# Performance work log

Hardware: AMD Instinct MI355X
Metric: run time of the kernel (lower is better)

Reference implementation:

```python
import jax, jax.numpy as jnp
import numpy as np

NMS_PRE_MAXSIZE = 4096
NMS_POST_MAXSIZE = 512
NMS_THRESH = 0.7


def setup_inputs() -> dict:
    key = jax.random.key(0)
    k1, k2, k3, k4, k5 = jax.random.split(key, 5)
    B, N, C = 4, 32768, 3
    # realistic 3D boxes: (x, y, z, dx, dy, dz, heading)
    xy = jax.random.uniform(k1, (B, N, 2), dtype=jnp.float32) * 70.0
    z = jax.random.uniform(k2, (B, N, 1), dtype=jnp.float32) * 4.0 - 2.0
    sizes = jax.random.uniform(k3, (B, N, 3), dtype=jnp.float32) * 3.0 + 1.0
    heading = jax.random.uniform(k4, (B, N, 1), dtype=jnp.float32) * 6.2832 - 3.1416
    batch_box_preds = jnp.concatenate([xy, z, sizes, heading], axis=-1)  # (B,N,7)
    batch_cls_preds = jax.random.uniform(k5, (B, N, C), dtype=jnp.float32)  # (B,N,3)
    return {"batch_box_preds": batch_box_preds, "batch_cls_preds": batch_cls_preds}


def _nms_single(boxes, scores, labels):
    # boxes (N,7), scores (N,), labels (N,) int32
    top_s, idx = jax.lax.top_k(scores, NMS_PRE_MAXSIZE)   # sort desc, keep pre-maxsize
    b = boxes[idx]                                        # (PRE,7)
    l = labels[idx]
    # BEV axis-aligned IoU (reference surrogate for the rotated-BEV CUDA IoU kernel)
    x, y, dx, dy = b[:, 0], b[:, 1], b[:, 3], b[:, 4]
    x1, x2 = x - 0.5 * dx, x + 0.5 * dx
    y1, y2 = y - 0.5 * dy, y + 0.5 * dy
    area = dx * dy
    ix = jnp.maximum(0.0, jnp.minimum(x2[:, None], x2[None, :]) - jnp.maximum(x1[:, None], x1[None, :]))
    iy = jnp.maximum(0.0, jnp.minimum(y2[:, None], y2[None, :]) - jnp.maximum(y1[:, None], y1[None, :]))
    inter = ix * iy
    iou = jax.lax.stop_gradient(inter / (area[:, None] + area[None, :] - inter + 1e-6))

    ar = jnp.arange(NMS_PRE_MAXSIZE)

    def body(i, keep):
        sup = (iou[i] > NMS_THRESH) & (ar > i) & keep[i]
        return keep & ~sup

    keep = jax.lax.fori_loop(0, NMS_PRE_MAXSIZE, body, jnp.ones(NMS_PRE_MAXSIZE, bool))

    # pack first NMS_POST_MAXSIZE kept boxes into fixed-size zero-padded outputs
    rank = jnp.cumsum(keep) - 1
    valid = keep & (rank < NMS_POST_MAXSIZE)
    pos = jnp.where(valid, rank, NMS_POST_MAXSIZE)  # invalid -> scratch row
    rois = jnp.zeros((NMS_POST_MAXSIZE + 1, 7), b.dtype).at[pos].set(b)[:NMS_POST_MAXSIZE]
    sc = jnp.zeros((NMS_POST_MAXSIZE + 1,), top_s.dtype).at[pos].set(top_s)[:NMS_POST_MAXSIZE]
    lb = jnp.zeros((NMS_POST_MAXSIZE + 1,), jnp.int32).at[pos].set(l)[:NMS_POST_MAXSIZE]
    return rois, sc, lb


def reference(batch_box_preds, batch_cls_preds):
    # per-box max score / argmax class (torch.max(cls_preds, dim=1) per sample)
    roi_scores_all = jnp.max(batch_cls_preds, axis=-1)                 # (B,N)
    roi_labels_all = jnp.argmax(batch_cls_preds, axis=-1).astype(jnp.int32)
    rois, roi_scores, roi_labels = jax.vmap(_nms_single)(batch_box_preds, roi_scores_all, roi_labels_all)
    return rois, roi_scores, roi_labels + 1  # labels shifted by +1 as in proposal_layer
```

## Files before the change

kernel.cpp:

```cpp
#include <hip/hip_runtime.h>
#include <stdint.h>

#define BB 4
#define NN 32768
#define PRE 4096
#define POST 512
#define NMS_TH 0.7f
#define MIDCAP 8192
#define P1G 10
#define T1 595
#define T2 1485

typedef unsigned long long u64;
typedef unsigned int u32;

__device__ __forceinline__ u32 orderable(float f) {
  u32 u = __float_as_uint(f);
  return (u & 0x80000000u) ? ~u : (u | 0x80000000u);
}
__device__ __forceinline__ float unorderable(u32 o) {
  u32 u = (o & 0x80000000u) ? (o & 0x7fffffffu) : ~o;
  return __uint_as_float(u);
}
__device__ __forceinline__ u32 bucket_of(float s) {
  u32 v = (u32)(s * 2147483648.0f);
  u32 bk = v >> 20;
  return bk > 2047u ? 2047u : bk;
}
__device__ __forceinline__ u64 readlane64(u64 v, int l) {
  u32 lo = (u32)__builtin_amdgcn_readlane((int)(u32)v, l);
  u32 hi = (u32)__builtin_amdgcn_readlane((int)(u32)(v >> 32), l);
  return ((u64)hi << 32) | lo;
}

__global__ void zero_kernel(u32* __restrict__ hist, u32* __restrict__ cnt_mid,
                            u64* __restrict__ rowAnyBm) {
  int t = blockIdx.x * 256 + threadIdx.x;
  if (t < BB * 2048) hist[t] = 0;
  if (t < BB * 64) rowAnyBm[t] = 0;
  if (t < BB) cnt_mid[t] = 0;
}

__global__ __launch_bounds__(256) void score_hist_kernel(const float* __restrict__ cls,
                                                         int* __restrict__ labels,
                                                         u64* __restrict__ keys,
                                                         u32* __restrict__ hist) {
  __shared__ u32 lh[2048];
  for (int t = threadIdx.x; t < 2048; t += 256) lh[t] = 0;
  __syncthreads();
  int t4 = blockIdx.x * 256 + threadIdx.x;
  int base4 = t4 * 4;
  const float4* c4 = (const float4*)(cls + (size_t)t4 * 12);
  float4 va = c4[0], vb = c4[1], vc = c4[2];
  float v[12] = {va.x, va.y, va.z, va.w, vb.x, vb.y, vb.z, vb.w, vc.x, vc.y, vc.z, vc.w};
  u64 ks[4]; int ls[4];
#pragma unroll
  for (int p = 0; p < 4; ++p) {
    float s = v[3 * p]; int l = 0;
    if (v[3 * p + 1] > s) { s = v[3 * p + 1]; l = 1; }
    if (v[3 * p + 2] > s) { s = v[3 * p + 2]; l = 2; }
    int n = (base4 + p) & (NN - 1);
    ks[p] = ((u64)orderable(s) << 32) | (u32)(~(u32)n);
    ls[p] = l;
    atomicAdd(&lh[bucket_of(s)], 1u);
  }
  *(ulonglong2*)(keys + base4) = make_ulonglong2(ks[0], ks[1]);
  *(ulonglong2*)(keys + base4 + 2) = make_ulonglong2(ks[2], ks[3]);
  *(int4*)(labels + base4) = make_int4(ls[0], ls[1], ls[2], ls[3]);
  __syncthreads();
  int b = blockIdx.x >> 5;
  for (int t = threadIdx.x; t < 2048; t += 256) {
    u32 vv = lh[t];
    if (vv) atomicAdd(&hist[b * 2048 + t], vv);
  }
}

__global__ __launch_bounds__(256) void select_kernel(const u32* __restrict__ hist,
                                                     u32* __restrict__ selinfo,
                                                     u32* __restrict__ sfxBuf,
                                                     u32* __restrict__ cursor) {
  __shared__ u32 sfx[2048];
  int b = blockIdx.x;
  for (int t = threadIdx.x; t < 2048; t += 256) sfx[t] = hist[b * 2048 + t];
  __syncthreads();
  for (int d = 1; d < 2048; d <<= 1) {
    u32 v[8];
#pragma unroll
    for (int i = 0; i < 8; ++i) {
      int t = threadIdx.x + i * 256;
      v[i] = (t + d < 2048) ? sfx[t + d] : 0;
    }
    __syncthreads();
#pragma unroll
    for (int i = 0; i < 8; ++i) sfx[threadIdx.x + i * 256] += v[i];
    __syncthreads();
  }
  for (int t = threadIdx.x; t < 2048; t += 256) {
    u32 above = (t + 1 < 2048) ? sfx[t + 1] : 0;
    sfxBuf[b * 2048 + t] = sfx[t];
    cursor[b * 2048 + t] = above;
    if (above < PRE && sfx[t] >= PRE) { selinfo[b * 2] = (u32)t; selinfo[b * 2 + 1] = above; }
  }
}

__global__ __launch_bounds__(256) void compact_kernel(const u64* __restrict__ keys,
                                                      const u32* __restrict__ selinfo,
                                                      u32* __restrict__ cursor,
                                                      u64* __restrict__ sel, u64* __restrict__ mid,
                                                      u32* __restrict__ cnt_mid) {
  int t4 = blockIdx.x * 256 + threadIdx.x;
  int base4 = t4 * 4;
  int b = base4 >> 15;
  u32 T = selinfo[b * 2];
  ulonglong2 k01 = *(const ulonglong2*)(keys + base4);
  ulonglong2 k23 = *(const ulonglong2*)(keys + base4 + 2);
  u64 kk[4] = {k01.x, k01.y, k23.x, k23.y};
#pragma unroll
  for (int p = 0; p < 4; ++p) {
    u64 key = kk[p];
    u32 bk = bucket_of(unorderable((u32)(key >> 32)));
    if (bk > T) {
      u32 q = atomicAdd(&cursor[b * 2048 + bk], 1u);
      sel[((size_t)b << 12) + q] = key;
    } else if (bk == T) {
      u32 q = atomicAdd(&cnt_mid[b], 1u);
      if (q < MIDCAP) mid[(size_t)b * MIDCAP + q] = key;
    }
  }
}

__global__ __launch_bounds__(64) void bsort_kernel(u64* __restrict__ sel, u64* __restrict__ mid,
                                                   const u32* __restrict__ sfxBuf,
                                                   const u32* __restrict__ selinfo,
                                                   const u32* __restrict__ cnt_mid,
                                                   const float* __restrict__ boxes,
                                                   const int* __restrict__ labels,
                                                   float* __restrict__ topBox,
                                                   float4* __restrict__ P,
                                                   float* __restrict__ AR,
                                                   float* __restrict__ topS,
                                                   int* __restrict__ topL) {
  int t = blockIdx.x & 2047;
  int b = blockIdx.x >> 11;
  int lane = threadIdx.x;
  u32 T = selinfo[b * 2];
  if ((u32)t < T) return;
  u64* selB = sel + ((size_t)b << 12);
  u32 start, end;
  if ((u32)t == T) {
    u32 C1 = selinfo[b * 2 + 1];
    int need = PRE - (int)C1;
    int M = (int)cnt_mid[b]; if (M > MIDCAP) M = MIDCAP;
    u64* midB = mid + (size_t)b * MIDCAP;
    for (int r = 0; r < need; ++r) {
      u64 best = 0; int bi = -1;
      for (int q = lane; q < M; q += 64) {
        u64 v = midB[q];
        if (v > best) { best = v; bi = q; }
      }
#pragma unroll
      for (int d = 32; d > 0; d >>= 1) {
        u64 ob = __shfl_xor(best, d, 64);
        int oi = __shfl_xor(bi, d, 64);
        if (ob > best) { best = ob; bi = oi; }
      }
      if (lane == 0) selB[C1 + r] = best;
      if (bi >= 0 && lane == (bi & 63)) midB[bi] = 0;
    }
    start = C1; end = PRE;
  } else {
    start = (t < 2047) ? sfxBuf[b * 2048 + t + 1] : 0u;
    end = sfxBuf[b * 2048 + t];
    int n = (int)(end - start);
    if (n > 64) {
      for (int r = 0; r < n - 1; ++r) {
        u64 best = 0; int bi = -1;
        for (int q = r + lane; q < n; q += 64) {
          u64 v = selB[start + q];
          if (v > best) { best = v; bi = q; }
        }
#pragma unroll
        for (int d = 32; d > 0; d >>= 1) {
          u64 ob = __shfl_xor(best, d, 64);
          int oi = __shfl_xor(bi, d, 64);
          if (ob > best) { best = ob; bi = oi; }
        }
        if (lane == 0) {
          u64 tmp = selB[start + r];
          selB[start + r] = best;
          selB[start + bi] = tmp;
        }
      }
    } else if (n > 1) {
      u64 v = (lane < n) ? selB[start + lane] : 0ULL;
#pragma unroll
      for (int k = 2; k <= 64; k <<= 1) {
#pragma unroll
        for (int j = k >> 1; j > 0; j >>= 1) {
          u64 o = __shfl_xor(v, j, 64);
          bool up = ((lane & k) == 0);
          bool first = ((lane & j) == 0);
          u64 mx = v > o ? v : o, mn = v > o ? o : v;
          v = (first == up) ? mx : mn;
        }
      }
      if (lane < n) selB[start + lane] = v;
    }
  }
  __builtin_amdgcn_s_waitcnt(0);
  for (u32 pos = start + lane; pos < end; pos += 64) {
    u64 key = selB[pos];
    u32 n = ~(u32)key;
    size_t src = (size_t)b * NN + n;
    const float* bx = boxes + src * 7;
    float x = bx[0], y = bx[1], dx = bx[3], dy = bx[4];
    size_t gidx = ((size_t)b << 12) + pos;
    float* tb = topBox + gidx * 7;
#pragma unroll
    for (int c = 0; c < 7; ++c) tb[c] = bx[c];
    float4 p;
    p.x = x - 0.5f * dx; p.z = x + 0.5f * dx;
    p.y = y - 0.5f * dy; p.w = y + 0.5f * dy;
    P[gidx] = p;
    AR[gidx] = dx * dy;
    topS[gidx] = unorderable((u32)(key >> 32));
    topL[gidx] = labels[src];
  }
}

__device__ __forceinline__ void mask_tile(int b, int rb, int w, int lane,
                                          const float4* __restrict__ P,
                                          const float* __restrict__ AR,
                                          u64* __restrict__ maskT,
                                          u64* __restrict__ diag,
                                          u64* __restrict__ rowAnyBm) {
  int base = b << 12;
  int row = (rb << 6) + lane;
  float4 rp = P[base + row];
  float rar = AR[base + row];
  const float4* __restrict__ Pcol = P + base + (w << 6);
  const float* __restrict__ ARcol = AR + base + (w << 6);
  u64 bits = 0;
  float margMin = 1.0f;
#pragma unroll 8
  for (int k = 0; k < 64; ++k) {
    float4 cb = Pcol[k];
    float ca = ARcol[k];
    float ix = fminf(rp.z, cb.z) - fmaxf(rp.x, cb.x); ix = fmaxf(0.0f, ix);
    float iy = fminf(rp.w, cb.w) - fmaxf(rp.y, cb.y); iy = fmaxf(0.0f, iy);
    float inter = ix * iy;
    float denom = ((rar + ca) - inter) + 1e-6f;
    float t = 0.7f * denom;
    bits |= ((u64)(inter > t ? 1u : 0u)) << k;
    margMin = fminf(margMin, fabsf(inter - t) - 2e-5f * t);
  }
  if (__any(margMin <= 0.0f)) {
    bits = 0;
    for (int k = 0; k < 64; ++k) {
      float4 cb = Pcol[k];
      float ca = ARcol[k];
      float ix = fminf(rp.z, cb.z) - fmaxf(rp.x, cb.x); ix = fmaxf(0.0f, ix);
      float iy = fminf(rp.w, cb.w) - fmaxf(rp.y, cb.y); iy = fmaxf(0.0f, iy);
      float inter = ix * iy;
      float denom = ((rar + ca) - inter) + 1e-6f;
      bits |= ((u64)(((inter / denom) > NMS_TH) ? 1u : 0u)) << k;
    }
  }
  maskT[((size_t)(b * 64 + w)) * PRE + row] = bits;
  if (w == rb) diag[base + row] = bits;
  else {
    u64 anyw = __ballot(bits != 0ULL);
    if (lane == 0 && anyw)
      atomicOr((unsigned long long*)&rowAnyBm[b * 64 + rb], anyw);
  }
}

__global__ __launch_bounds__(256) void mask1_kernel(const float4* __restrict__ P,
                                                    const float* __restrict__ AR,
                                                    u64* __restrict__ maskT,
                                                    u64* __restrict__ diag,
                                                    u64* __restrict__ rowAnyBm) {
  int b = blockIdx.y;
  int ti = blockIdx.x * 4 + (threadIdx.x >> 6);
  if (ti >= T1) return;
  int lane = threadIdx.x & 63;
  int rb = 0;
  while (rb < P1G - 1 && (64 * (rb + 1) - ((rb + 1) * rb) / 2) <= ti) ++rb;
  int w = rb + (ti - (64 * rb - (rb * (rb - 1)) / 2));
  mask_tile(b, rb, w, lane, P, AR, maskT, diag, rowAnyBm);
}

__global__ __launch_bounds__(256) void mask2_kernel(const float4* __restrict__ P,
                                                    const float* __restrict__ AR,
                                                    u64* __restrict__ maskT,
                                                    u64* __restrict__ diag,
                                                    u64* __restrict__ rowAnyBm,
                                                    const u32* __restrict__ doneFlag) {
  int b = blockIdx.y;
  if (doneFlag[b]) return;
  int ti = blockIdx.x * 4 + (threadIdx.x >> 6);
  if (ti >= T2) return;
  int lane = threadIdx.x & 63;
  int R = 64 - P1G;
  int rr = 0;
  while (rr < R - 1 && (R * (rr + 1) - ((rr + 1) * rr) / 2) <= ti) ++rr;
  int rb = rr + P1G;
  int w = rb + (ti - (R * rr - (rr * (rr - 1)) / 2));
  mask_tile(b, rb, w, lane, P, AR, maskT, diag, rowAnyBm);
}

__global__ __launch_bounds__(64, 1) void scan_kernel(const u64* __restrict__ maskT,
                                                     const u64* __restrict__ diag,
                                                     const u64* __restrict__ rowAnyBm,
                                                     const float* __restrict__ topBox,
                                                     const float* __restrict__ topS,
                                                     const int* __restrict__ topL,
                                                     float* __restrict__ out,
                                                     u64* __restrict__ rState,
                                                     u64* __restrict__ kwState,
                                                     u32* __restrict__ nkState,
                                                     u32* __restrict__ doneFlag,
                                                     int phase) {
  __shared__ u64 kwLDS[64];
  __shared__ u64 dgLDS[(64 - P1G) * 64];
  int b = blockIdx.x;
  int lane = threadIdx.x;
  if (phase == 1 && doneFlag[b]) return;
  const u64* m = maskT + (size_t)b * 64 * PRE;
  const u64* dg = diag + (size_t)b * PRE;
  u64 rowAnyW = rowAnyBm[b * 64 + lane];
  u64 r; int nk, gs, ge;
  if (phase == 0) {
    kwLDS[lane] = 0; r = 0; nk = 0; gs = 0; ge = P1G;
  } else {
    kwLDS[lane] = (lane < P1G) ? kwState[b * 64 + lane] : 0;
    r = rState[b * 64 + lane]; nk = nkState[b]; gs = P1G; ge = 64;
  }
  for (int t = lane; t < (ge - gs) * 64; t += 64) dgLDS[t] = dg[(size_t)gs * 64 + t];
  __syncthreads();
  bool done = false;
  for (int g = gs; g < ge; ++g) {
    u64 d_cur = dgLDS[(g - gs) * 64 + lane];
    u64 aboveMask = ~((2ULL << lane) - 1ULL);
    u64 rem = __ballot((d_cur & aboveMask) != 0ULL);
    u64 sup = readlane64(r, g);
    if (rem) {
      do {
        int k = __ffsll((long long)rem) - 1;
        rem &= rem - 1;
        if (!((sup >> k) & 1ULL))
          sup |= readlane64(d_cur, k) & ~((2ULL << k) - 1ULL);
      } while (rem);
    }
    u64 keep = ~sup;
    u64 need = keep & readlane64(rowAnyW, g);
    if (need) {
      u64 accr = 0;
      do {
        int t = __ffsll((long long)need) - 1;
        need &= need - 1;
        accr |= m[(size_t)lane * PRE + (size_t)(g << 6) + t];
      } while (need);
      r |= accr;
    }
    if (lane == 0) kwLDS[g] = keep;
    nk += (int)__popcll(keep);
    if (nk >= POST) { done = true; break; }
  }
  __syncthreads();
  if (phase == 0 && !done) {
    rState[b * 64 + lane] = r;
    if (lane < P1G) kwState[b * 64 + lane] = kwLDS[lane];
    if (lane == 0) { nkState[b] = nk; doneFlag[b] = 0; }
    return;
  }
  if (phase == 0 && lane == 0) doneFlag[b] = 1;
  u64 kw = kwLDS[lane];
  int cnt = __popcll(kw);
  int pfx = cnt;
#pragma unroll
  for (int d = 1; d < 64; d <<= 1) {
    int up = __shfl_up(pfx, d, 64);
    if (lane >= d) pfx += up;
  }
  int total = __shfl(pfx, 63, 64);
  int pos = pfx - cnt;
  float* outR = out;
  float* outS = out + BB * POST * 7;
  float* outL = outS + BB * POST;
  while (kw) {
    int t = __ffsll((long long)kw) - 1;
    kw &= kw - 1;
    if (pos < POST) {
      int i = (lane << 6) + t;
      int g = (b << 9) + pos;
      const float* tb = topBox + ((size_t)(b << 12) + i) * 7;
#pragma unroll
      for (int c = 0; c < 7; ++c) outR[(size_t)g * 7 + c] = tb[c];
      outS[g] = topS[(b << 12) + i];
      outL[g] = (float)(topL[(b << 12) + i] + 1);
    }
    ++pos;
  }
  int fin = total < POST ? total : POST;
  for (int s = fin + lane; s < POST; s += 64) {
    int g = (b << 9) + s;
#pragma unroll
    for (int c = 0; c < 7; ++c) outR[(size_t)g * 7 + c] = 0.0f;
    outS[g] = 0.0f;
    outL[g] = 1.0f;
  }
}

extern "C" void kernel_launch(void* const* d_in, const int* in_sizes, int n_in,
                              void* d_out, int out_size, void* d_ws, size_t ws_size,
                              hipStream_t stream) {
  const float* boxes = (const float*)d_in[0];
  const float* cls   = (const float*)d_in[1];
  float* out = (float*)d_out;

  char* p = (char*)d_ws;
  auto take = [&](size_t bytes) { char* r = p; p += (bytes + 255) & ~(size_t)255; return (void*)r; };
  u64*   keys    = (u64*)  take((size_t)BB * NN * 8);
  int*   labels  = (int*)  take((size_t)BB * NN * 4);
  u32*   hist    = (u32*)  take((size_t)BB * 2048 * 4);
  u32*   selinfo = (u32*)  take((size_t)BB * 2 * 4);
  u32*   sfxBuf  = (u32*)  take((size_t)BB * 2048 * 4);
  u32*   cursor  = (u32*)  take((size_t)BB * 2048 * 4);
  u32*   cnt_mid = (u32*)  take((size_t)BB * 4);
  u64*   sel     = (u64*)  take((size_t)BB * PRE * 8);
  u64*   mid     = (u64*)  take((size_t)BB * MIDCAP * 8);
  float* topBox  = (float*)take((size_t)BB * PRE * 7 * 4);
  float4* Pb     = (float4*)take((size_t)BB * PRE * 16);
  float* AR      = (float*)take((size_t)BB * PRE * 4);
  float* topS    = (float*)take((size_t)BB * PRE * 4);
  int*   topL    = (int*)  take((size_t)BB * PRE * 4);
  u64*   maskT   = (u64*)  take((size_t)BB * 64 * PRE * 8);
  u64*   diagBuf = (u64*)  take((size_t)BB * PRE * 8);
  u64*   rowAny  = (u64*)  take((size_t)BB * 64 * 8);
  u64*   rState  = (u64*)  take((size_t)BB * 64 * 8);
  u64*   kwState = (u64*)  take((size_t)BB * 64 * 8);
  u32*   nkState = (u32*)  take((size_t)BB * 4);
  u32*   doneFlg = (u32*)  take((size_t)BB * 4);

  zero_kernel<<<32, 256, 0, stream>>>(hist, cnt_mid, rowAny);
  score_hist_kernel<<<BB * NN / 1024, 256, 0, stream>>>(cls, labels, keys, hist);
  select_kernel<<<BB, 256, 0, stream>>>(hist, selinfo, sfxBuf, cursor);
  compact_kernel<<<BB * NN / 1024, 256, 0, stream>>>(keys, selinfo, cursor, sel, mid, cnt_mid);
  bsort_kernel<<<BB * 2048, 64, 0, stream>>>(sel, mid, sfxBuf, selinfo, cnt_mid,
                                             boxes, labels, topBox, Pb, AR, topS, topL);
  mask1_kernel<<<dim3((T1 + 3) / 4, BB), 256, 0, stream>>>(Pb, AR, maskT, diagBuf, rowAny);
  scan_kernel<<<BB, 64, 0, stream>>>(maskT, diagBuf, rowAny, topBox, topS, topL, out,
                                     rState, kwState, nkState, doneFlg, 0);
  mask2_kernel<<<dim3((T2 + 3) / 4, BB), 256, 0, stream>>>(Pb, AR, maskT, diagBuf, rowAny, doneFlg);
  scan_kernel<<<BB, 64, 0, stream>>>(maskT, diagBuf, rowAny, topBox, topS, topL, out,
                                     rState, kwState, nkState, doneFlg, 1);
}
```

Measured before the change: 85.90 us.

## Fuse select and scan stages into producers via last-block-done counters

Replaces the global histogram atomics with per-block partial histograms, and lets the last block of each batch reduce them and run the suffix scan. This removes the separate select kernel. The mask1/mask2 kernels likewise use per-batch atomic counters so the last finishing block runs the corresponding scan phase inline, removing two scan kernel launches. The scan's diag preload now uses all 256 threads. The trade-off is extra threadfences and a serial tail done by one block per batch, plus a larger partial-histogram buffer.

```diff
diff --git a/kernel.cpp b/kernel.cpp
--- a/kernel.cpp
+++ b/kernel.cpp
@@ -10,6 +10,8 @@
 #define P1G 10
 #define T1 595
 #define T2 1485
+#define T1B ((T1 + 3) / 4)
+#define T2B ((T2 + 3) / 4)
 
 typedef unsigned long long u64;
 typedef unsigned int u32;
@@ -33,19 +35,24 @@
   return ((u64)hi << 32) | lo;
 }
 
-__global__ void zero_kernel(u32* __restrict__ hist, u32* __restrict__ cnt_mid,
-                            u64* __restrict__ rowAnyBm) {
-  int t = blockIdx.x * 256 + threadIdx.x;
-  if (t < BB * 2048) hist[t] = 0;
+__global__ void zero_kernel(u32* __restrict__ cnt_mid, u64* __restrict__ rowAnyBm,
+                            u32* __restrict__ ctrSel, u32* __restrict__ ctrM1,
+                            u32* __restrict__ ctrM2) {
+  int t = threadIdx.x;
   if (t < BB * 64) rowAnyBm[t] = 0;
-  if (t < BB) cnt_mid[t] = 0;
-}
-
-__global__ __launch_bounds__(256) void score_hist_kernel(const float* __restrict__ cls,
-                                                         int* __restrict__ labels,
-                                                         u64* __restrict__ keys,
-                                                         u32* __restrict__ hist) {
+  if (t < BB) { cnt_mid[t] = 0; ctrSel[t] = 0; ctrM1[t] = 0; ctrM2[t] = 0; }
+}
+
+__global__ __launch_bounds__(256) void score_hist_sel_kernel(const float* __restrict__ cls,
+                                                             int* __restrict__ labels,
+                                                             u64* __restrict__ keys,
+                                                             u32* __restrict__ histP,
+                                                             u32* __restrict__ ctrSel,
+                                                             u32* __restrict__ selinfo,
+                                                             u32* __restrict__ sfxBuf,
+                                                             u32* __restrict__ cursor) {
   __shared__ u32 lh[2048];
+  __shared__ int lastSh;
   for (int t = threadIdx.x; t < 2048; t += 256) lh[t] = 0;
   __syncthreads();
   int t4 = blockIdx.x * 256 + threadIdx.x;
@@ -69,37 +76,42 @@
   *(int4*)(labels + base4) = make_int4(ls[0], ls[1], ls[2], ls[3]);
   __syncthreads();
   int b = blockIdx.x >> 5;
+  u32* myrow = histP + (size_t)blockIdx.x * 2048;
+  for (int t = threadIdx.x; t < 2048; t += 256) myrow[t] = lh[t];
+  __threadfence();
+  __syncthreads();
+  if (threadIdx.x == 0) {
+    u32 old = atomicAdd(&ctrSel[b], 1u);
+    lastSh = (old == 31);
+  }
+  __syncthreads();
+  if (!lastSh) return;
+  __threadfence();
   for (int t = threadIdx.x; t < 2048; t += 256) {
-    u32 vv = lh[t];
-    if (vv) atomicAdd(&hist[b * 2048 + t], vv);
-  }
-}
-
-__global__ __launch_bounds__(256) void select_kernel(const u32* __restrict__ hist,
-                                                     u32* __restrict__ selinfo,
-                                                     u32* __restrict__ sfxBuf,
-                                                     u32* __restrict__ cursor) {
-  __shared__ u32 sfx[2048];
-  int b = blockIdx.x;
-  for (int t = threadIdx.x; t < 2048; t += 256) sfx[t] = hist[b * 2048 + t];
+    u32 s = 0;
+    const u32* pp = histP + (size_t)(b * 32) * 2048 + t;
+#pragma unroll
+    for (int j = 0; j < 32; ++j) s += pp[(size_t)j * 2048];
+    lh[t] = s;
+  }
   __syncthreads();
   for (int d = 1; d < 2048; d <<= 1) {
-    u32 v[8];
+    u32 vv[8];
 #pragma unroll
     for (int i = 0; i < 8; ++i) {
       int t = threadIdx.x + i * 256;
-      v[i] = (t + d < 2048) ? sfx[t + d] : 0;
+      vv[i] = (t + d < 2048) ? lh[t + d] : 0;
     }
     __syncthreads();
 #pragma unroll
-    for (int i = 0; i < 8; ++i) sfx[threadIdx.x + i * 256] += v[i];
+    for (int i = 0; i < 8; ++i) lh[threadIdx.x + i * 256] += vv[i];
     __syncthreads();
   }
   for (int t = threadIdx.x; t < 2048; t += 256) {
-    u32 above = (t + 1 < 2048) ? sfx[t + 1] : 0;
-    sfxBuf[b * 2048 + t] = sfx[t];
+    u32 above = (t + 1 < 2048) ? lh[t + 1] : 0;
+    sfxBuf[b * 2048 + t] = lh[t];
     cursor[b * 2048 + t] = above;
-    if (above < PRE && sfx[t] >= PRE) { selinfo[b * 2] = (u32)t; selinfo[b * 2 + 1] = above; }
+    if (above < PRE && lh[t] >= PRE) { selinfo[b * 2] = (u32)t; selinfo[b * 2 + 1] = above; }
   }
 }
 
@@ -275,69 +287,34 @@
   }
 }
 
-__global__ __launch_bounds__(256) void mask1_kernel(const float4* __restrict__ P,
-                                                    const float* __restrict__ AR,
-                                                    u64* __restrict__ maskT,
-                                                    u64* __restrict__ diag,
-                                                    u64* __restrict__ rowAnyBm) {
-  int b = blockIdx.y;
-  int ti = blockIdx.x * 4 + (threadIdx.x >> 6);
-  if (ti >= T1) return;
-  int lane = threadIdx.x & 63;
-  int rb = 0;
-  while (rb < P1G - 1 && (64 * (rb + 1) - ((rb + 1) * rb) / 2) <= ti) ++rb;
-  int w = rb + (ti - (64 * rb - (rb * (rb - 1)) / 2));
-  mask_tile(b, rb, w, lane, P, AR, maskT, diag, rowAnyBm);
-}
-
-__global__ __launch_bounds__(256) void mask2_kernel(const float4* __restrict__ P,
-                                                    const float* __restrict__ AR,
-                                                    u64* __restrict__ maskT,
-                                                    u64* __restrict__ diag,
-                                                    u64* __restrict__ rowAnyBm,
-                                                    const u32* __restrict__ doneFlag) {
-  int b = blockIdx.y;
-  if (doneFlag[b]) return;
-  int ti = blockIdx.x * 4 + (threadIdx.x >> 6);
-  if (ti >= T2) return;
-  int lane = threadIdx.x & 63;
-  int R = 64 - P1G;
-  int rr = 0;
-  while (rr < R - 1 && (R * (rr + 1) - ((rr + 1) * rr) / 2) <= ti) ++rr;
-  int rb = rr + P1G;
-  int w = rb + (ti - (R * rr - (rr * (rr - 1)) / 2));
-  mask_tile(b, rb, w, lane, P, AR, maskT, diag, rowAnyBm);
-}
-
-__global__ __launch_bounds__(64, 1) void scan_kernel(const u64* __restrict__ maskT,
-                                                     const u64* __restrict__ diag,
-                                                     const u64* __restrict__ rowAnyBm,
-                                                     const float* __restrict__ topBox,
-                                                     const float* __restrict__ topS,
-                                                     const int* __restrict__ topL,
-                                                     float* __restrict__ out,
-                                                     u64* __restrict__ rState,
-                                                     u64* __restrict__ kwState,
-                                                     u32* __restrict__ nkState,
-                                                     u32* __restrict__ doneFlag,
-                                                     int phase) {
-  __shared__ u64 kwLDS[64];
-  __shared__ u64 dgLDS[(64 - P1G) * 64];
-  int b = blockIdx.x;
-  int lane = threadIdx.x;
-  if (phase == 1 && doneFlag[b]) return;
+__device__ __forceinline__ void scan_phase(int b, int phase,
+                                           const u64* __restrict__ maskT,
+                                           const u64* __restrict__ diag,
+                                           const u64* __restrict__ rowAnyBm,
+                                           const float* __restrict__ topBox,
+                                           const float* __restrict__ topS,
+                                           const int* __restrict__ topL,
+                                           float* __restrict__ out,
+                                           u64* __restrict__ rState,
+                                           u64* __restrict__ kwState,
+                                           u32* __restrict__ nkState,
+                                           u32* __restrict__ doneFlag,
+                                           u64* kwLDS, u64* dgLDS) {
+  int tid = threadIdx.x;
   const u64* m = maskT + (size_t)b * 64 * PRE;
   const u64* dg = diag + (size_t)b * PRE;
+  int gs = (phase == 0) ? 0 : P1G;
+  int ge = (phase == 0) ? P1G : 64;
+  if (tid < 64) kwLDS[tid] = (phase == 0) ? 0ULL
+                           : ((tid < P1G) ? kwState[b * 64 + tid] : 0ULL);
+  for (int t = tid; t < (ge - gs) * 64; t += 256) dgLDS[t] = dg[(size_t)gs * 64 + t];
+  __syncthreads();
+  if (tid >= 64) return;
+  int lane = tid;
   u64 rowAnyW = rowAnyBm[b * 64 + lane];
-  u64 r; int nk, gs, ge;
-  if (phase == 0) {
-    kwLDS[lane] = 0; r = 0; nk = 0; gs = 0; ge = P1G;
-  } else {
-    kwLDS[lane] = (lane < P1G) ? kwState[b * 64 + lane] : 0;
-    r = rState[b * 64 + lane]; nk = nkState[b]; gs = P1G; ge = 64;
-  }
-  for (int t = lane; t < (ge - gs) * 64; t += 64) dgLDS[t] = dg[(size_t)gs * 64 + t];
-  __syncthreads();
+  u64 r; int nk;
+  if (phase == 0) { r = 0; nk = 0; }
+  else { r = rState[b * 64 + lane]; nk = nkState[b]; }
   bool done = false;
   for (int g = gs; g < ge; ++g) {
     u64 d_cur = dgLDS[(g - gs) * 64 + lane];
@@ -367,7 +344,6 @@
     nk += (int)__popcll(keep);
     if (nk >= POST) { done = true; break; }
   }
-  __syncthreads();
   if (phase == 0 && !done) {
     rState[b * 64 + lane] = r;
     if (lane < P1G) kwState[b * 64 + lane] = kwLDS[lane];
@@ -412,6 +388,87 @@
   }
 }
 
+__global__ __launch_bounds__(256) void mask1_scan_kernel(const float4* __restrict__ P,
+                                                         const float* __restrict__ AR,
+                                                         u64* __restrict__ maskT,
+                                                         u64* __restrict__ diag,
+                                                         u64* __restrict__ rowAnyBm,
+                                                         u32* __restrict__ ctrM1,
+                                                         const float* __restrict__ topBox,
+                                                         const float* __restrict__ topS,
+                                                         const int* __restrict__ topL,
+                                                         float* __restrict__ out,
+                                                         u64* __restrict__ rState,
+                                                         u64* __restrict__ kwState,
+                                                         u32* __restrict__ nkState,
+                                                         u32* __restrict__ doneFlag) {
+  __shared__ u64 kwLDS[64];
+  __shared__ u64 dgLDS[P1G * 64];
+  __shared__ int lastSh;
+  int b = blockIdx.y;
+  int ti = blockIdx.x * 4 + (threadIdx.x >> 6);
+  int lane = threadIdx.x & 63;
+  if (ti < T1) {
+    int rb = 0;
+    while (rb < P1G - 1 && (64 * (rb + 1) - ((rb + 1) * rb) / 2) <= ti) ++rb;
+    int w = rb + (ti - (64 * rb - (rb * (rb - 1)) / 2));
+    mask_tile(b, rb, w, lane, P, AR, maskT, diag, rowAnyBm);
+  }
+  __threadfence();
+  __syncthreads();
+  if (threadIdx.x == 0) {
+    u32 old = atomicAdd(&ctrM1[b], 1u);
+    lastSh = (old == (u32)(gridDim.x - 1));
+  }
+  __syncthreads();
+  if (!lastSh) return;
+  __threadfence();
+  scan_phase(b, 0, maskT, diag, rowAnyBm, topBox, topS, topL, out,
+             rState, kwState, nkState, doneFlag, kwLDS, dgLDS);
+}
+
+__global__ __launch_bounds__(256) void mask2_scan_kernel(const float4* __restrict__ P,
+                                                         const float* __restrict__ AR,
+                                                         u64* __restrict__ maskT,
+                                                         u64* __restrict__ diag,
+                                                         u64* __restrict__ rowAnyBm,
+                                                         u32* __restrict__ ctrM2,
+                                                         const float* __restrict__ topBox,
+                                                         const float* __restrict__ topS,
+                                                         const int* __restrict__ topL,
+                                                         float* __restrict__ out,
+                                                         u64* __restrict__ rState,
+                                                         u64* __restrict__ kwState,
+                                                         u32* __restrict__ nkState,
+                                                         u32* __restrict__ doneFlag) {
+  __shared__ u64 kwLDS[64];
+  __shared__ u64 dgLDS[(64 - P1G) * 64];
+  __shared__ int lastSh;
+  int b = blockIdx.y;
+  if (doneFlag[b]) return;
+  int ti = blockIdx.x * 4 + (threadIdx.x >> 6);
+  int lane = threadIdx.x & 63;
+  if (ti < T2) {
+    int R = 64 - P1G;
+    int rr = 0;
+    while (rr < R - 1 && (R * (rr + 1) - ((rr + 1) * rr) / 2) <= ti) ++rr;
+    int rb = rr + P1G;
+    int w = rb + (ti - (R * rr - (rr * (rr - 1)) / 2));
+    mask_tile(b, rb, w, lane, P, AR, maskT, diag, rowAnyBm);
+  }
+  __threadfence();
+  __syncthreads();
+  if (threadIdx.x == 0) {
+    u32 old = atomicAdd(&ctrM2[b], 1u);
+    lastSh = (old == (u32)(gridDim.x - 1));
+  }
+  __syncthreads();
+  if (!lastSh) return;
+  __threadfence();
+  scan_phase(b, 1, maskT, diag, rowAnyBm, topBox, topS, topL, out,
+             rState, kwState, nkState, doneFlag, kwLDS, dgLDS);
+}
+
 extern "C" void kernel_launch(void* const* d_in, const int* in_sizes, int n_in,
                               void* d_out, int out_size, void* d_ws, size_t ws_size,
                               hipStream_t stream) {
@@ -423,7 +480,7 @@
   auto take = [&](size_t bytes) { char* r = p; p += (bytes + 255) & ~(size_t)255; return (void*)r; };
   u64*   keys    = (u64*)  take((size_t)BB * NN * 8);
   int*   labels  = (int*)  take((size_t)BB * NN * 4);
-  u32*   hist    = (u32*)  take((size_t)BB * 2048 * 4);
+  u32*   histP   = (u32*)  take((size_t)BB * 32 * 2048 * 4);
   u32*   selinfo = (u32*)  take((size_t)BB * 2 * 4);
   u32*   sfxBuf  = (u32*)  take((size_t)BB * 2048 * 4);
   u32*   cursor  = (u32*)  take((size_t)BB * 2048 * 4);
@@ -442,17 +499,20 @@
   u64*   kwState = (u64*)  take((size_t)BB * 64 * 8);
   u32*   nkState = (u32*)  take((size_t)BB * 4);
   u32*   doneFlg = (u32*)  take((size_t)BB * 4);
-
-  zero_kernel<<<32, 256, 0, stream>>>(hist, cnt_mid, rowAny);
-  score_hist_kernel<<<BB * NN / 1024, 256, 0, stream>>>(cls, labels, keys, hist);
-  select_kernel<<<BB, 256, 0, stream>>>(hist, selinfo, sfxBuf, cursor);
+  u32*   ctrSel  = (u32*)  take((size_t)BB * 4);
+  u32*   ctrM1   = (u32*)  take((size_t)BB * 4);
+  u32*   ctrM2   = (u32*)  take((size_t)BB * 4);
+
+  zero_kernel<<<1, 256, 0, stream>>>(cnt_mid, rowAny, ctrSel, ctrM1, ctrM2);
+  score_hist_sel_kernel<<<BB * NN / 1024, 256, 0, stream>>>(cls, labels, keys, histP,
+                                                            ctrSel, selinfo, sfxBuf, cursor);
   compact_kernel<<<BB * NN / 1024, 256, 0, stream>>>(keys, selinfo, cursor, sel, mid, cnt_mid);
   bsort_kernel<<<BB * 2048, 64, 0, stream>>>(sel, mid, sfxBuf, selinfo, cnt_mid,
                                              boxes, labels, topBox, Pb, AR, topS, topL);
-  mask1_kernel<<<dim3((T1 + 3) / 4, BB), 256, 0, stream>>>(Pb, AR, maskT, diagBuf, rowAny);
-  scan_kernel<<<BB, 64, 0, stream>>>(maskT, diagBuf, rowAny, topBox, topS, topL, out,
-                                     rState, kwState, nkState, doneFlg, 0);
-  mask2_kernel<<<dim3((T2 + 3) / 4, BB), 256, 0, stream>>>(Pb, AR, maskT, diagBuf, rowAny, doneFlg);
-  scan_kernel<<<BB, 64, 0, stream>>>(maskT, diagBuf, rowAny, topBox, topS, topL, out,
-                                     rState, kwState, nkState, doneFlg, 1);
-}
+  mask1_scan_kernel<<<dim3(T1B, BB), 256, 0, stream>>>(Pb, AR, maskT, diagBuf, rowAny, ctrM1,
+                                                       topBox, topS, topL, out,
+                                                       rState, kwState, nkState, doneFlg);
+  mask2_scan_kernel<<<dim3(T2B, BB), 256, 0, stream>>>(Pb, AR, maskT, diagBuf, rowAny, ctrM2,
+                                                       topBox, topS, topL, out,
+                                                       rState, kwState, nkState, doneFlg);
+}
```

After: 140.3 us. 1.63x slower.
